# Performance work log

Measured on AMD Instinct MI355X. Metric: run time of the kernel, lower is better.

The kernel has to match this reference:

```python
import jax, jax.numpy as jnp
from jax import lax
import numpy as np

RPN_BBOX_STD_DEV = np.array([0.1, 0.1, 0.2, 0.2], dtype=np.float32)
PRE_NMS_LIMIT = 2048      # anchors kept before NMS (sorted by score)
NUM_PROPOSAL = 1000       # post-NMS proposal count (init kwarg num_proposal)
NMS_THRESHOLD = 0.7       # init kwarg nms_threshold


def setup_inputs() -> dict:
    key = jax.random.key(0)
    k1, k2, k3, k4, k5, k6 = jax.random.split(key, 6)
    B, N = 4, 1_000_000
    rpn_probs = jax.random.uniform(k1, (B, N, 2), dtype=jnp.float32)
    rpn_bbox = jax.random.normal(k2, (B, N, 4), dtype=jnp.float32)
    # well-formed normalized anchors (y1, x1, y2, x2)
    cy = jax.random.uniform(k3, (B, N), dtype=jnp.float32)
    cx = jax.random.uniform(k4, (B, N), dtype=jnp.float32)
    h = jax.random.uniform(k5, (B, N), dtype=jnp.float32) * 0.25 + 0.05
    w = jax.random.uniform(k6, (B, N), dtype=jnp.float32) * 0.25 + 0.05
    anchors = jnp.stack([cy - 0.5 * h, cx - 0.5 * w, cy + 0.5 * h, cx + 0.5 * w], axis=-1)
    return {"rpn_probs": rpn_probs, "rpn_bbox": rpn_bbox, "anchors": anchors}


def apply_box_deltas(boxes, deltas):
    # boxes: (..., 4) as (y1, x1, y2, x2); deltas: (dy, dx, log(dh), log(dw))
    h = boxes[..., 2] - boxes[..., 0]
    w = boxes[..., 3] - boxes[..., 1]
    cy = boxes[..., 0] + 0.5 * h + deltas[..., 0] * h
    cx = boxes[..., 1] + 0.5 * w + deltas[..., 1] * w
    h = h * jnp.exp(deltas[..., 2])
    w = w * jnp.exp(deltas[..., 3])
    return jnp.stack([cy - 0.5 * h, cx - 0.5 * w, cy + 0.5 * h, cx + 0.5 * w], axis=-1)


def pairwise_iou(boxes):
    # boxes: (P, 4) -> (P, P)
    y1, x1, y2, x2 = boxes[:, 0], boxes[:, 1], boxes[:, 2], boxes[:, 3]
    area = (y2 - y1) * (x2 - x1)
    ih = jnp.maximum(jnp.minimum(y2[:, None], y2[None, :]) - jnp.maximum(y1[:, None], y1[None, :]), 0.0)
    iw = jnp.maximum(jnp.minimum(x2[:, None], x2[None, :]) - jnp.maximum(x1[:, None], x1[None, :]), 0.0)
    inter = ih * iw
    union = area[:, None] + area[None, :] - inter
    return inter / (union + 1e-8)


def nms_single(boxes):
    # boxes (P, 4) sorted by score desc; greedy NMS then pad/clip to NUM_PROPOSAL
    P = boxes.shape[0]
    iou = pairwise_iou(boxes)
    idx = jnp.arange(P)

    def body(keep, i):
        suppress = keep[i] & (iou[i] > NMS_THRESHOLD) & (idx > i)
        return keep & ~suppress, None

    keep, _ = lax.scan(body, jnp.ones((P,), jnp.bool_), idx)
    rank = jnp.cumsum(keep) - 1                      # position among kept boxes
    valid = keep & (rank < NUM_PROPOSAL)
    pos = jnp.where(valid, rank, NUM_PROPOSAL)       # overflow row dropped below
    out = jnp.zeros((NUM_PROPOSAL + 1, 4), boxes.dtype).at[pos].set(
        jnp.where(valid[:, None], boxes, 0.0))
    return out[:NUM_PROPOSAL]


def reference(rpn_probs, rpn_bbox, anchors):
    scores = rpn_probs[:, :, 1]                                  # foreground prob (B, N)
    deltas = rpn_bbox * jnp.asarray(RPN_BBOX_STD_DEV)
    _, ix = lax.top_k(scores, PRE_NMS_LIMIT)                     # (B, P)
    deltas_top = jnp.take_along_axis(deltas, ix[..., None], axis=1)
    anchors_top = jnp.take_along_axis(anchors, ix[..., None], axis=1)
    boxes = apply_box_deltas(anchors_top, deltas_top)            # (B, P, 4)
    boxes = jnp.clip(boxes, 0.0, 1.0)                            # clip to [0,1] window
    proposals = jax.vmap(nms_single)(boxes)                      # (B, NUM_PROPOSAL, 4)
    return proposals
```

## Files before the change

kernel.cpp:

```cpp
#include <hip/hip_runtime.h>

#define B_ 4
#define N_ 1000000
#define K_ 2048
#define P_ 1000
#define CAP_ 8192
#define THR_ 0.7f
#define NF4_ 500000
#define META_STRIDE 32
#define TILE_ 512
#define NCH_ (CAP_ / TILE_)
#define NSTAGE 448
#define CROW 1536

#define OFF_HIST 0
#define OFF_META 1048576
#define OFF_COARSE 1049600
#define OFF_ROWANY 1053696
#define OFF_CAND 1054720
#define OFF_BOX  1316864
#define OFF_MASK 1447936

__device__ __forceinline__ unsigned fkey(float f) {
  unsigned u = __float_as_uint(f);
  return (u & 0x80000000u) ? ~u : (u | 0x80000000u);
}

__device__ __forceinline__ unsigned long long readlane64(unsigned long long v, int l) {
  unsigned lo = (unsigned)__builtin_amdgcn_readlane((int)(unsigned)(v & 0xffffffffull), l);
  unsigned hi = (unsigned)__builtin_amdgcn_readlane((int)(unsigned)(v >> 32), l);
  return ((unsigned long long)hi << 32) | (unsigned long long)lo;
}

#define PIN16(k) asm volatile("" : "+v"(k[0]), "+v"(k[1]), "+v"(k[2]), "+v"(k[3]), \
                                   "+v"(k[4]), "+v"(k[5]), "+v"(k[6]), "+v"(k[7]), \
                                   "+v"(k[8]), "+v"(k[9]), "+v"(k[10]), "+v"(k[11]), \
                                   "+v"(k[12]), "+v"(k[13]), "+v"(k[14]), "+v"(k[15]))

__global__ void __launch_bounds__(1024) hist_kernel(const float4* __restrict__ probs4,
                                                    unsigned* __restrict__ hist) {
  int b = blockIdx.y;
  __shared__ unsigned h[32768];
  for (int i = threadIdx.x; i < 32768; i += 1024) h[i] = 0u;
  __syncthreads();
  const float4* p4 = probs4 + (size_t)b * NF4_;
  int base = blockIdx.x * 8192;
  float4 v[8];
#pragma unroll
  for (int c = 0; c < 8; ++c) {
    int i4 = base + c * 1024 + threadIdx.x;
    v[c] = (i4 < NF4_) ? p4[i4] : make_float4(0.f, 0.f, 0.f, 0.f);
  }
  unsigned k[16];
#pragma unroll
  for (int c = 0; c < 8; ++c) { k[2 * c] = fkey(v[c].y) >> 16; k[2 * c + 1] = fkey(v[c].w) >> 16; }
  PIN16(k);
#pragma unroll
  for (int c = 0; c < 8; ++c) {
    int i4 = base + c * 1024 + threadIdx.x;
    if (i4 < NF4_) {
      unsigned b0 = k[2 * c], b1 = k[2 * c + 1];
      atomicAdd(&h[b0 >> 1], 1u << ((b0 & 1u) << 4));
      atomicAdd(&h[b1 >> 1], 1u << ((b1 & 1u) << 4));
    }
  }
  __syncthreads();
  unsigned* g = hist + ((size_t)b << 16);
  for (int w = threadIdx.x; w < 32768; w += 1024) {
    unsigned x = h[w];
    if (x) {
      unsigned c0 = x & 0xFFFFu, c1 = x >> 16;
      if (c0) atomicAdd(&g[2 * w], c0);
      if (c1) atomicAdd(&g[2 * w + 1], c1);
    }
  }
}

__global__ void __launch_bounds__(64) coarse_kernel(const unsigned* __restrict__ hist,
                                                    unsigned* __restrict__ coarse) {
  int b = blockIdx.y, g = blockIdx.x, lane = threadIdx.x;
  const uint4* h4 = (const uint4*)(hist + (((size_t)b) << 16) + ((size_t)g << 8));
  uint4 v = h4[lane];
  unsigned s = v.x + v.y + v.z + v.w;
#pragma unroll
  for (int off = 32; off >= 1; off >>= 1) s += __shfl_xor(s, off, 64);
  if (lane == 0) coarse[b * 256 + g] = s;
}

__global__ void select_kernel(const unsigned* __restrict__ hist, const unsigned* __restrict__ coarse,
                              unsigned* __restrict__ meta) {
  int b = blockIdx.x, t = threadIdx.x;
  __shared__ unsigned suf[256];
  __shared__ int tc_s;
  __shared__ unsigned above_s;
  const unsigned* g = hist + ((size_t)b << 16);
  suf[t] = coarse[b * 256 + t];
  __syncthreads();
  for (int off = 1; off < 256; off <<= 1) {
    unsigned add = (t + off < 256) ? suf[t + off] : 0u;
    __syncthreads();
    suf[t] += add;
    __syncthreads();
  }
  unsigned nxt = (t < 255) ? suf[t + 1] : 0u;
  if (suf[t] >= K_ && (t == 255 || nxt < K_)) { tc_s = t; above_s = nxt; }
  __syncthreads();
  int tc = tc_s;
  unsigned above = above_s;
  unsigned bs = g[tc * 256 + t];
  __syncthreads();
  suf[t] = bs;
  __syncthreads();
  for (int off = 1; off < 256; off <<= 1) {
    unsigned add = (t + off < 256) ? suf[t + off] : 0u;
    __syncthreads();
    suf[t] += add;
    __syncthreads();
  }
  unsigned nxt2 = (t < 255) ? suf[t + 1] : 0u;
  if (above + suf[t] >= K_ && (t == 255 || above + nxt2 < K_))
    meta[b * META_STRIDE + 0] = (unsigned)(tc * 256 + t);
}

__global__ void __launch_bounds__(256) compact_kernel(const float4* __restrict__ probs4,
                                                      unsigned* __restrict__ meta,
                                                      uint2* __restrict__ cand) {
  int b = blockIdx.y;
  __shared__ unsigned lcnt, gbase_s;
  __shared__ uint2 buf[4096];
  if (threadIdx.x == 0) lcnt = 0u;
  __syncthreads();
  unsigned cb = meta[b * META_STRIDE + 0];
  const float4* p4 = probs4 + (size_t)b * NF4_;
  int base = blockIdx.x * 2048;
  int lane = threadIdx.x & 63;
  float4 v[8];
#pragma unroll
  for (int c = 0; c < 8; ++c) {
    int i4 = base + c * 256 + threadIdx.x;
    v[c] = (i4 < NF4_) ? p4[i4] : make_float4(0.f, 0.f, 0.f, 0.f);
  }
  unsigned k[16];
#pragma unroll
  for (int c = 0; c < 8; ++c) { k[2 * c] = fkey(v[c].y); k[2 * c + 1] = fkey(v[c].w); }
  PIN16(k);
#pragma unroll
  for (int c = 0; c < 8; ++c) {
#pragma unroll
    for (int s = 0; s < 2; ++s) {
      int i4 = base + c * 256 + threadIdx.x;
      unsigned key = k[2 * c + s];
      bool pass = (i4 < NF4_) && ((key >> 16) >= cb);
      unsigned long long m = __ballot(pass);
      if (m) {
        int leader = __ffsll(m) - 1;
        unsigned wbase = 0;
        if (lane == leader) wbase = atomicAdd(&lcnt, (unsigned)__popcll(m));
        wbase = __shfl(wbase, leader, 64);
        if (pass) {
          unsigned pos = wbase + (unsigned)__popcll(m & ((1ull << lane) - 1ull));
          buf[pos] = make_uint2(key, (unsigned)(2 * i4 + s));
        }
      }
    }
  }
  __syncthreads();
  unsigned cnt = lcnt;
  if (threadIdx.x == 0) gbase_s = atomicAdd(&meta[b * META_STRIDE + 1], cnt);
  __syncthreads();
  unsigned gbase = gbase_s;
  for (unsigned i = threadIdx.x; i < cnt; i += 256) {
    unsigned pos = gbase + i;
    if (pos < CAP_) cand[(size_t)b * CAP_ + pos] = buf[i];
  }
}

__global__ void __launch_bounds__(256) rank_kernel(const uint2* __restrict__ cand,
                                                   const unsigned* __restrict__ meta,
                                                   unsigned* __restrict__ partial) {
  int b = blockIdx.z;
  unsigned M = meta[b * META_STRIDE + 1];
  if (M > CAP_) M = CAP_;
  unsigned tb = blockIdx.y * TILE_;
  if (tb >= M) return;
  if ((unsigned)(blockIdx.x * 256) >= M) return;
  __shared__ __align__(16) uint2 tile[TILE_];
  unsigned n = M - tb;
  if (n > TILE_) n = TILE_;
  for (unsigned t = threadIdx.x; t < n; t += 256) tile[t] = cand[(size_t)b * CAP_ + tb + t];
  int ci = blockIdx.x * 256 + threadIdx.x;
  bool act = ci < (int)M;
  uint2 me = make_uint2(0u, 0u);
  if (act) me = cand[(size_t)b * CAP_ + ci];
  unsigned long long my = ((unsigned long long)me.x << 32) | (unsigned long long)(unsigned)(~me.y);
  __syncthreads();
  if (act) {
    unsigned rank = 0;
    unsigned n2 = n >> 1;
    const uint4* t4 = (const uint4*)tile;
    for (unsigned j = 0; j < n2; ++j) {
      uint4 v = t4[j];
      unsigned long long c0 = ((unsigned long long)v.x << 32) | (unsigned long long)(unsigned)(~v.y);
      unsigned long long c1 = ((unsigned long long)v.z << 32) | (unsigned long long)(unsigned)(~v.w);
      rank += (unsigned)(c0 > my) + (unsigned)(c1 > my);
    }
    if (n & 1) {
      uint2 v = tile[n - 1];
      unsigned long long c0 = ((unsigned long long)v.x << 32) | (unsigned long long)(unsigned)(~v.y);
      rank += (unsigned)(c0 > my);
    }
    partial[((size_t)b * NCH_ + blockIdx.y) * CAP_ + ci] = rank;
  }
}

__global__ void __launch_bounds__(256) scatter_kernel(const uint2* __restrict__ cand,
                                                      const unsigned* __restrict__ meta,
                                                      const unsigned* __restrict__ partial,
                                                      const float4* __restrict__ bbox,
                                                      const float4* __restrict__ anch,
                                                      float4* __restrict__ boxes) {
  int b = blockIdx.y;
  unsigned M = meta[b * META_STRIDE + 1];
  if (M > CAP_) M = CAP_;
  unsigned ci = blockIdx.x * 256 + threadIdx.x;
  if (ci >= M) return;
  unsigned nch = (M + TILE_ - 1) / TILE_;
  const unsigned* pp = partial + (size_t)b * NCH_ * CAP_ + ci;
  unsigned rank = 0;
  for (unsigned c = 0; c < nch; ++c) rank += pp[(size_t)c * CAP_];
  if (rank >= K_) return;
  unsigned idx = cand[(size_t)b * CAP_ + ci].y;
  size_t base = (size_t)b * N_ + idx;
  float4 a = anch[base];
  float4 d = bbox[base];
  float d0 = d.x * 0.1f, d1 = d.y * 0.1f, d2 = d.z * 0.2f, d3 = d.w * 0.2f;
  float h = a.z - a.x, w = a.w - a.y;
  float cy = (a.x + 0.5f * h) + d0 * h;
  float cx = (a.y + 0.5f * w) + d1 * w;
  float h2 = h * expf(d2);
  float w2 = w * expf(d3);
  float y1 = cy - 0.5f * h2, x1 = cx - 0.5f * w2;
  float y2 = cy + 0.5f * h2, x2 = cx + 0.5f * w2;
  y1 = fminf(fmaxf(y1, 0.f), 1.f);
  x1 = fminf(fmaxf(x1, 0.f), 1.f);
  y2 = fminf(fmaxf(y2, 0.f), 1.f);
  x2 = fminf(fmaxf(x2, 0.f), 1.f);
  boxes[(b << 11) + rank] = make_float4(y1, x1, y2, x2);
}

__global__ void mask_kernel(const float4* __restrict__ boxes, unsigned long long* __restrict__ mask,
                            unsigned long long* __restrict__ rowAny) {
  int wid = blockIdx.x * 4 + (threadIdx.x >> 6);
  int lane = threadIdx.x & 63;
  int b = wid >> 12;
  int rb = (wid >> 5) & 127;
  int jb = wid & 31;
  if (jb < (rb >> 2)) return;
  int j = (jb << 6) + lane;
  float4 bj = boxes[(b << 11) + j];
  float areaJ = (bj.z - bj.x) * (bj.w - bj.y);
#pragma unroll
  for (int r = 0; r < 16; ++r) {
    int i = (rb << 4) + r;
    float4 bi = boxes[(b << 11) + i];
    float areaI = (bi.z - bi.x) * (bi.w - bi.y);
    float yA = fmaxf(bi.x, bj.x), xA = fmaxf(bi.y, bj.y);
    float yB = fminf(bi.z, bj.z), xB = fminf(bi.w, bj.w);
    float ih = fmaxf(yB - yA, 0.f), iw = fmaxf(xB - xA, 0.f);
    float inter = ih * iw;
    float uni = areaI + areaJ - inter;
    float iou = inter / (uni + 1e-8f);
    bool pred = (iou > THR_) && (j > i);
    unsigned long long bits = __ballot(pred);
    if (lane == 0) {
      mask[((size_t)((b << 11) + i) << 5) + jb] = bits;
      if (bits) atomicOr(&rowAny[b * 32 + (i >> 6)], 1ull << (i & 63));
    }
  }
}

__global__ void __launch_bounds__(256) nms_kernel(const unsigned long long* __restrict__ mask,
                                                  const unsigned long long* __restrict__ rowAny,
                                                  const float4* __restrict__ boxes,
                                                  float4* __restrict__ out) {
  int b = blockIdx.x;
  int t = threadIdx.x;
  int w = t & 31, g = t >> 5;
  __shared__ unsigned long long rowsBuf[NSTAGE][32];
  __shared__ unsigned short evRow[2048];
  __shared__ unsigned long long supA[32], supB[32];
  __shared__ int pre[32];
  __shared__ short sel[P_];
  __shared__ int E_s, EC_s, chg_s, cnt_s;
  for (int r = t; r < P_; r += 256) sel[r] = -1;
  if (t < 32) { supA[t] = 0ull; supB[t] = 0ull; }
  if (t == 0) { E_s = 0; EC_s = 0; chg_s = 0; }
  if (t < 64) {
    unsigned long long anyv = (t < 32) ? rowAny[b * 32 + t] : 0ull;
    unsigned pc = (unsigned)__popcll(anyv);
    unsigned pref = pc;
#pragma unroll
    for (int off = 1; off < 32; off <<= 1) {
      unsigned tv = __shfl_up(pref, off, 64);
      if ((t & 31) >= off) pref += tv;
    }
    if (t == 31) E_s = (int)pref;
    if (t == 23) EC_s = (int)pref;
    if (t < 32) {
      unsigned o = pref - pc;
      unsigned long long bm = anyv;
      while (bm) {
        int i = __ffsll((long long)bm) - 1;
        bm &= bm - 1;
        evRow[o++] = (unsigned short)((t << 6) + i);
      }
    }
  }
  __syncthreads();
  int E = E_s, EC = EC_s;
  const unsigned long long* mb = mask + (((size_t)(b << 11)) << 5);
  int ns = (E < NSTAGE) ? E : NSTAGE;
  for (int base = 0; base < ns; base += 64) {
    unsigned long long v[8];
#pragma unroll
    for (int j = 0; j < 8; ++j) {
      int e = base + j * 8 + g;
      v[j] = 0ull;
      if (e < ns) {
        int r = (int)evRow[e];
        if (w >= (r >> 6)) v[j] = mb[((size_t)r << 5) + w];
      }
    }
#pragma unroll
    for (int j = 0; j < 8; ++j) {
      int e = base + j * 8 + g;
      if (e < ns) rowsBuf[e][w] = v[j];
    }
  }
  __syncthreads();
  unsigned long long* cur = supA;
  unsigned long long* nxt = supB;
  int limit = EC;
  for (;;) {
    unsigned long long acc = 0ull;
    for (int e = g; e < limit; e += 8) {
      int r = (int)evRow[e];
      int rw = r >> 6;
      if (w >= rw) {
        unsigned long long sw = cur[rw];
        if (!((sw >> (r & 63)) & 1ull))
          acc |= (e < NSTAGE) ? rowsBuf[e][w] : mb[((size_t)r << 5) + w];
      }
    }
    if (acc) atomicOr((unsigned long long*)&nxt[w], acc);
    __syncthreads();
    if (t < 32) {
      if (t == 0) chg_s = 0;
      if (nxt[t] != cur[t]) chg_s = 1;
      cur[t] = 0ull;
    }
    __syncthreads();
    { unsigned long long* tmp = cur; cur = nxt; nxt = tmp; }
    if (chg_s) continue;
    if (limit >= E) break;
    if (t == 0) {
      int c = 0;
      for (int i = 0; i < 24; ++i) c += (int)__popcll(cur[i]);
      cnt_s = CROW - c;
    }
    __syncthreads();
    if (cnt_s >= P_) break;
    limit = E;
  }
  if (t == 0) {
    int run = 0;
    for (int c = 0; c < 32; ++c) { pre[c] = run; run += (int)__popcll(~cur[c]); }
  }
  __syncthreads();
  for (int i = t; i < K_; i += 256) {
    int c = i >> 6, k2 = i & 63;
    unsigned long long km = ~cur[c];
    if ((km >> k2) & 1ull) {
      int rank = pre[c] + (int)__popcll(km & ((1ull << k2) - 1ull));
      if (rank < P_) sel[rank] = (short)i;
    }
  }
  __syncthreads();
  for (int r = t; r < P_; r += 256) {
    int i = sel[r];
    float4 v = make_float4(0.f, 0.f, 0.f, 0.f);
    if (i >= 0) v = boxes[(b << 11) + i];
    out[b * P_ + r] = v;
  }
}

extern "C" void kernel_launch(void* const* d_in, const int* in_sizes, int n_in,
                              void* d_out, int out_size, void* d_ws, size_t ws_size,
                              hipStream_t stream) {
  const float4* probs4 = (const float4*)d_in[0];
  const float4* bbox   = (const float4*)d_in[1];
  const float4* anch   = (const float4*)d_in[2];
  char* ws = (char*)d_ws;
  unsigned* hist = (unsigned*)(ws + OFF_HIST);
  unsigned* meta = (unsigned*)(ws + OFF_META);
  unsigned* coarse = (unsigned*)(ws + OFF_COARSE);
  unsigned long long* rowAny = (unsigned long long*)(ws + OFF_ROWANY);
  uint2* cand = (uint2*)(ws + OFF_CAND);
  float4* boxes = (float4*)(ws + OFF_BOX);
  unsigned long long* mask = (unsigned long long*)(ws + OFF_MASK);
  unsigned* partial = (unsigned*)(ws + OFF_MASK);
  float4* out = (float4*)d_out;

  hipMemsetAsync(ws, 0, OFF_CAND, stream);

  hist_kernel<<<dim3(62, B_), 1024, 0, stream>>>(probs4, hist);
  coarse_kernel<<<dim3(256, B_), 64, 0, stream>>>(hist, coarse);
  select_kernel<<<B_, 256, 0, stream>>>(hist, coarse, meta);
  compact_kernel<<<dim3(245, B_), 256, 0, stream>>>(probs4, meta, cand);
  rank_kernel<<<dim3(CAP_ / 256, NCH_, B_), 256, 0, stream>>>(cand, meta, partial);
  scatter_kernel<<<dim3(CAP_ / 256, B_), 256, 0, stream>>>(cand, meta, partial, bbox, anch, boxes);
  mask_kernel<<<(B_ * 128 * 32) / 4, 256, 0, stream>>>(boxes, mask, rowAny);
  nms_kernel<<<B_, 256, 0, stream>>>(mask, rowAny, boxes, out);
}
```

Baseline: 250.8 us.

## Replace iterative fixed-point NMS with single-wave sequential greedy scan using readlane

```diff
diff --git a/kernel.cpp b/kernel.cpp
--- a/kernel.cpp
+++ b/kernel.cpp
@@ -10,7 +10,7 @@
 #define META_STRIDE 32
 #define TILE_ 512
 #define NCH_ (CAP_ / TILE_)
-#define NSTAGE 448
+#define NSTAGE 576
 #define CROW 1536
 
 #define OFF_HIST 0
@@ -279,6 +279,29 @@
   }
 }
 
+__device__ __forceinline__ void scan_global(const unsigned long long* __restrict__ mb,
+                                            const unsigned short* evR, int from, int to,
+                                            int w, unsigned long long& sup) {
+  for (int base = from; base < to; base += 16) {
+    int ra[16];
+    unsigned long long va[16];
+#pragma unroll
+    for (int j = 0; j < 16; ++j) ra[j] = (base + j < to) ? (int)evR[base + j] : 0;
+#pragma unroll
+    for (int j = 0; j < 16; ++j) {
+      va[j] = 0ull;
+      if (base + j < to && w >= (ra[j] >> 6)) va[j] = mb[((size_t)ra[j] << 5) + w];
+    }
+#pragma unroll
+    for (int j = 0; j < 16; ++j) {
+      if (base + j < to) {
+        unsigned long long sw = readlane64(sup, ra[j] >> 6);
+        if (!((sw >> (ra[j] & 63)) & 1ull)) sup |= va[j];
+      }
+    }
+  }
+}
+
 __global__ void __launch_bounds__(256) nms_kernel(const unsigned long long* __restrict__ mask,
                                                   const unsigned long long* __restrict__ rowAny,
                                                   const float4* __restrict__ boxes,
@@ -288,13 +311,13 @@
   int w = t & 31, g = t >> 5;
   __shared__ unsigned long long rowsBuf[NSTAGE][32];
   __shared__ unsigned short evRow[2048];
-  __shared__ unsigned long long supA[32], supB[32];
+  __shared__ unsigned long long supSh[32];
   __shared__ int pre[32];
   __shared__ short sel[P_];
-  __shared__ int E_s, EC_s, chg_s, cnt_s;
+  __shared__ int E_s, EC_s;
   for (int r = t; r < P_; r += 256) sel[r] = -1;
-  if (t < 32) { supA[t] = 0ull; supB[t] = 0ull; }
-  if (t == 0) { E_s = 0; EC_s = 0; chg_s = 0; }
+  if (t == 0) { E_s = 0; EC_s = 0; }
+  __syncthreads();
   if (t < 64) {
     unsigned long long anyv = (t < 32) ? rowAny[b * 32 + t] : 0ull;
     unsigned pc = (unsigned)__popcll(anyv);
@@ -319,17 +342,16 @@
   __syncthreads();
   int E = E_s, EC = EC_s;
   const unsigned long long* mb = mask + (((size_t)(b << 11)) << 5);
-  int ns = (E < NSTAGE) ? E : NSTAGE;
+  int ns = (EC < NSTAGE) ? EC : NSTAGE;
   for (int base = 0; base < ns; base += 64) {
     unsigned long long v[8];
+    int rr[8];
 #pragma unroll
     for (int j = 0; j < 8; ++j) {
       int e = base + j * 8 + g;
+      rr[j] = (e < ns) ? (int)evRow[e] : 0;
       v[j] = 0ull;
-      if (e < ns) {
-        int r = (int)evRow[e];
-        if (w >= (r >> 6)) v[j] = mb[((size_t)r << 5) + w];
-      }
+      if (e < ns && w >= (rr[j] >> 6)) v[j] = mb[((size_t)rr[j] << 5) + w];
     }
 #pragma unroll
     for (int j = 0; j < 8; ++j) {
@@ -338,48 +360,49 @@
     }
   }
   __syncthreads();
-  unsigned long long* cur = supA;
-  unsigned long long* nxt = supB;
-  int limit = EC;
-  for (;;) {
-    unsigned long long acc = 0ull;
-    for (int e = g; e < limit; e += 8) {
-      int r = (int)evRow[e];
-      int rw = r >> 6;
-      if (w >= rw) {
-        unsigned long long sw = cur[rw];
-        if (!((sw >> (r & 63)) & 1ull))
-          acc |= (e < NSTAGE) ? rowsBuf[e][w] : mb[((size_t)r << 5) + w];
+  if (t < 64) {
+    unsigned long long sup = 0ull;
+    unsigned long long va[16], vb[16];
+    int ra[16], rb[16];
+#pragma unroll
+    for (int j = 0; j < 16; ++j) {
+      ra[j] = (j < ns) ? (int)evRow[j] : 0;
+      va[j] = (j < ns) ? rowsBuf[j][w] : 0ull;
+    }
+    for (int base = 0; base < ns; base += 16) {
+#pragma unroll
+      for (int j = 0; j < 16; ++j) {
+        int e = base + 16 + j;
+        rb[j] = (e < ns) ? (int)evRow[e] : 0;
+        vb[j] = (e < ns) ? rowsBuf[e][w] : 0ull;
       }
-    }
-    if (acc) atomicOr((unsigned long long*)&nxt[w], acc);
-    __syncthreads();
-    if (t < 32) {
-      if (t == 0) chg_s = 0;
-      if (nxt[t] != cur[t]) chg_s = 1;
-      cur[t] = 0ull;
-    }
-    __syncthreads();
-    { unsigned long long* tmp = cur; cur = nxt; nxt = tmp; }
-    if (chg_s) continue;
-    if (limit >= E) break;
-    if (t == 0) {
-      int c = 0;
-      for (int i = 0; i < 24; ++i) c += (int)__popcll(cur[i]);
-      cnt_s = CROW - c;
-    }
-    __syncthreads();
-    if (cnt_s >= P_) break;
-    limit = E;
-  }
+#pragma unroll
+      for (int j = 0; j < 16; ++j) {
+        if (base + j < ns) {
+          unsigned long long sw = readlane64(sup, ra[j] >> 6);
+          if (!((sw >> (ra[j] & 63)) & 1ull)) sup |= va[j];
+        }
+      }
+#pragma unroll
+      for (int j = 0; j < 16; ++j) { ra[j] = rb[j]; va[j] = vb[j]; }
+    }
+    if (ns < EC) scan_global(mb, evRow, ns, EC, w, sup);
+    unsigned cnt = (w < 24) ? (unsigned)__popcll(~sup) : 0u;
+#pragma unroll
+    for (int off = 1; off < 64; off <<= 1) cnt += __shfl_xor(cnt, off, 64);
+    cnt >>= 1;
+    if ((int)cnt < P_ && EC < E) scan_global(mb, evRow, EC, E, w, sup);
+    if (t < 32) supSh[w] = sup;
+  }
+  __syncthreads();
   if (t == 0) {
     int run = 0;
-    for (int c = 0; c < 32; ++c) { pre[c] = run; run += (int)__popcll(~cur[c]); }
+    for (int c = 0; c < 32; ++c) { pre[c] = run; run += (int)__popcll(~supSh[c]); }
   }
   __syncthreads();
   for (int i = t; i < K_; i += 256) {
     int c = i >> 6, k2 = i & 63;
-    unsigned long long km = ~cur[c];
+    unsigned long long km = ~supSh[c];
     if ((km >> k2) & 1ull) {
       int rank = pre[c] + (int)__popcll(km & ((1ull << k2) - 1ull));
       if (rank < P_) sel[rank] = (short)i;
```

Measured after the change: 252.6 us. No clear change (+0.7%).
